# Optimization experiments

Hardware: AMD Instinct MI355X
Metric: run time of the kernel (lower is better)

## Reference

```python
import jax, jax.numpy as jnp
import numpy as np

TEMPERATURE = 30.0
LN_EPS = 1e-5

B, CIN, COUT, S, HID, K = 64, 256, 512, 4096, 64, 4


def setup_inputs() -> dict:
    key = jax.random.key(0)
    ks = jax.random.split(key, 4)
    x = jax.random.normal(ks[0], (B, CIN, S), dtype=jnp.float32)
    w1 = jax.random.normal(ks[1], (HID, CIN), dtype=jnp.float32) * (1.0 / np.sqrt(CIN))
    w2 = jax.random.normal(ks[2], (K, HID), dtype=jnp.float32) * (1.0 / np.sqrt(HID))
    b2 = jnp.zeros((K,), dtype=jnp.float32)
    conv_w = jax.random.normal(ks[3], (K, COUT, CIN), dtype=jnp.float32) * (1.0 / np.sqrt(CIN))
    conv_b = jnp.zeros((K, COUT), dtype=jnp.float32)
    gamma = jnp.ones((S,), dtype=jnp.float32)
    beta = jnp.zeros((S,), dtype=jnp.float32)
    return {"x": x, "w1": w1, "w2": w2, "b2": b2, "conv_w": conv_w,
            "conv_b": conv_b, "gamma": gamma, "beta": beta}


def reference(x, w1, w2, b2, conv_w, conv_b, gamma, beta):
    # --- attention over K kernel experts (global avg pool -> FC -> ReLU -> FC -> softmax/T) ---
    pooled = x.mean(axis=-1)                               # [B, Cin]
    h = jax.nn.relu(pooled @ w1.T)                         # [B, H]
    logits = h @ w2.T + b2                                 # [B, K]
    att = jax.nn.softmax(logits / TEMPERATURE, axis=-1)    # [B, K]
    # --- per-sample mixed 1x1 conv weights (grouped-conv trick == batched matmul) ---
    Wb = jnp.einsum('bk,koi->boi', att, conv_w)            # [B, Cout, Cin]
    bb = att @ conv_b                                      # [B, Cout]
    y = jnp.einsum('boi,bis->bos', Wb, x) + bb[:, :, None]  # [B, Cout, S]
    # --- LayerNorm over time axis (Samples) ---
    mu = y.mean(axis=-1, keepdims=True)
    var = y.var(axis=-1, keepdims=True)
    y = (y - mu) * jax.lax.rsqrt(var + LN_EPS) * gamma + beta
    # --- GELU (torch default: exact erf); dropout is identity in eval mode ---
    return jax.nn.gelu(y, approximate=False)
```

## Files before the change

kernel.cpp:

```cpp
#include <hip/hip_runtime.h>
#include <hip/hip_bf16.h>

#define B_   64
#define CIN  256
#define COUT 512
#define S_   4096
#define HID  64
#define KEXP 4

typedef float f32x4 __attribute__((ext_vector_type(4)));
typedef short bf16x8 __attribute__((ext_vector_type(8)));

static __device__ __forceinline__ unsigned short f2bf(float f) {
    union { float f; unsigned u; } c; c.f = f;
    unsigned r = c.u + 0x7FFFu + ((c.u >> 16) & 1u);
    return (unsigned short)(r >> 16);
}
static __device__ __forceinline__ float bf2f(unsigned short u) {
    union { unsigned u; float f; } c; c.u = ((unsigned)u) << 16;
    return c.f;
}

#define GSTR 68
__global__ __launch_bounds__(512, 2) void k_gram_part(const float* __restrict__ x,
                                                      unsigned short* __restrict__ part,
                                                      float* __restrict__ ppart,
                                                      unsigned short* __restrict__ xF) {
    __shared__ unsigned short lds[256 * GSTR];
    int bid = blockIdx.x;
    int b = bid & 63, sc = bid >> 6;
    int t = threadIdx.x, lane = t & 63, wv = t >> 6;
    int wr = wv >> 1, wc = wv & 1;
    const float* xb = x + (size_t)b * CIN * S_;
    unsigned short* xFb = xF + (size_t)b * S_ * CIN;

    f32x4 acc[4][8] = {};
    float psum[8] = {0.f, 0.f, 0.f, 0.f, 0.f, 0.f, 0.f, 0.f};

    for (int step = 0; step < 16; ++step) {
        int s0 = sc * 1024 + step * 64;
        __syncthreads();
#pragma unroll
        for (int p = 0; p < 8; ++p) {
            int i = t + p * 512;
            int row = i >> 4, f4 = i & 15;
            float4 v = *(const float4*)(xb + (size_t)row * S_ + s0 + f4 * 4);
            psum[p] += v.x + v.y + v.z + v.w;
            unsigned short u[4] = {f2bf(v.x), f2bf(v.y), f2bf(v.z), f2bf(v.w)};
            *(uint2*)&lds[row * GSTR + f4 * 4] = *(const uint2*)u;
        }
        __syncthreads();
        {
#pragma unroll
            for (int it = 0; it < 4; ++it) {
                int slot = t + it * 512;
                int chunk = slot >> 6;
                int st_l = chunk >> 3, kb = chunk & 7;
                int l = slot & 63;
                unsigned short tmp[8];
#pragma unroll
                for (int j = 0; j < 8; ++j)
                    tmp[j] = lds[(kb * 32 + (l >> 4) * 8 + j) * GSTR + st_l * 16 + (l & 15)];
                *(uint4*)(xFb + ((size_t)((s0 >> 4) + st_l) * 8 + kb) * 512 + l * 8) = *(const uint4*)tmp;
            }
        }
#pragma unroll
        for (int kk = 0; kk < 2; ++kk) {
            bf16x8 bfr[8];
#pragma unroll
            for (int nf = 0; nf < 8; ++nf)
                bfr[nf] = *(const bf16x8*)&lds[(wc * 128 + nf * 16 + (lane & 15)) * GSTR + kk * 32 + (lane >> 4) * 8];
#pragma unroll
            for (int mfi = 0; mfi < 4; ++mfi) {
                bf16x8 afr = *(const bf16x8*)&lds[(wr * 64 + mfi * 16 + (lane & 15)) * GSTR + kk * 32 + (lane >> 4) * 8];
#pragma unroll
                for (int nf = 0; nf < 8; ++nf)
                    acc[mfi][nf] = __builtin_amdgcn_mfma_f32_16x16x32_bf16(afr, bfr[nf], acc[mfi][nf], 0, 0, 0);
            }
        }
    }
#pragma unroll
    for (int p = 0; p < 8; ++p) {
        float s = psum[p];
        s += __shfl_xor(s, 1); s += __shfl_xor(s, 2);
        s += __shfl_xor(s, 4); s += __shfl_xor(s, 8);
        if ((t & 15) == 0) ppart[((size_t)sc * 64 + b) * 256 + ((t + p * 512) >> 4)] = s;
    }
    unsigned short* pb = part + ((size_t)sc * 64 + b) * 65536;
#pragma unroll
    for (int mfi = 0; mfi < 4; ++mfi) {
#pragma unroll
        for (int r = 0; r < 4; ++r) {
            int row = wr * 64 + mfi * 16 + (lane >> 4) * 4 + r;
#pragma unroll
            for (int nf = 0; nf < 8; ++nf)
                pb[row * 256 + wc * 128 + nf * 16 + (lane & 15)] = f2bf(acc[mfi][nf][r]);
        }
    }
}

__global__ __launch_bounds__(256) void k_gred(const unsigned short* __restrict__ part,
                                              const float* __restrict__ ppart,
                                              unsigned short* __restrict__ ghat,
                                              float* __restrict__ pooled) {
    int b = blockIdx.x, t = threadIdx.x;
    const size_t bo = (size_t)b * 65536;
    const size_t scs = (size_t)64 * 65536;
    const float inv = 1.f / S_;
    for (int it = 0; it < 32; ++it) {
        size_t i = bo + (size_t)(it * 256 + t) * 8;
        union { uint4 v; unsigned short s[8]; } a0, a1, a2, a3, o;
        a0.v = *(const uint4*)(part + i);
        a1.v = *(const uint4*)(part + scs + i);
        a2.v = *(const uint4*)(part + 2 * scs + i);
        a3.v = *(const uint4*)(part + 3 * scs + i);
#pragma unroll
        for (int j = 0; j < 8; ++j)
            o.s[j] = f2bf((bf2f(a0.s[j]) + bf2f(a1.s[j]) + bf2f(a2.s[j]) + bf2f(a3.s[j])) * inv);
        *(uint4*)&ghat[i] = o.v;
    }
    float p = ppart[(size_t)b * 256 + t] + ppart[(size_t)(64 + b) * 256 + t]
            + ppart[(size_t)(128 + b) * 256 + t] + ppart[(size_t)(192 + b) * 256 + t];
    pooled[b * 256 + t] = p * inv;
}

__global__ __launch_bounds__(64) void k_att(const float* __restrict__ pooled,
                                            const float* __restrict__ w1,
                                            const float* __restrict__ w2,
                                            const float* __restrict__ b2,
                                            float* __restrict__ att_out) {
    int b = blockIdx.x, t = threadIdx.x;
    __shared__ float pl[CIN];
    __shared__ float hl[HID];
    __shared__ float satt[KEXP];
    for (int j = t; j < CIN; j += 64) pl[j] = pooled[b * CIN + j];
    __syncthreads();
    float acc = 0.f;
    const float* w1r = w1 + t * CIN;
#pragma unroll 4
    for (int c = 0; c < CIN; c += 4) {
        float4 w = *(const float4*)(w1r + c);
        acc += w.x * pl[c] + w.y * pl[c + 1] + w.z * pl[c + 2] + w.w * pl[c + 3];
    }
    hl[t] = fmaxf(acc, 0.f);
    __syncthreads();
    if (t < KEXP) {
        float a = 0.f;
        for (int j = 0; j < HID; ++j) a += hl[j] * w2[t * HID + j];
        satt[t] = (a + b2[t]) * (1.0f / 30.0f);
    }
    __syncthreads();
    if (t == 0) {
        float m = fmaxf(fmaxf(satt[0], satt[1]), fmaxf(satt[2], satt[3]));
        float e0 = expf(satt[0] - m), e1 = expf(satt[1] - m);
        float e2 = expf(satt[2] - m), e3 = expf(satt[3] - m);
        float inv = 1.f / (e0 + e1 + e2 + e3);
        att_out[b * KEXP + 0] = e0 * inv;
        att_out[b * KEXP + 1] = e1 * inv;
        att_out[b * KEXP + 2] = e2 * inv;
        att_out[b * KEXP + 3] = e3 * inv;
    }
}

__global__ __launch_bounds__(256) void k_wb(const float* __restrict__ conv_w,
                                            const float* __restrict__ att,
                                            unsigned short* __restrict__ wb) {
    int bid = blockIdx.x;
    int b = bid >> 5, o0 = (bid & 31) * 16;
    int t = threadIdx.x;
    int o = o0 + (t >> 4);
    int i0 = (t & 15) * 16;
    float ak[KEXP];
#pragma unroll
    for (int k = 0; k < KEXP; ++k) ak[k] = att[b * KEXP + k];
    float acc[16];
#pragma unroll
    for (int j = 0; j < 16; ++j) acc[j] = 0.f;
#pragma unroll
    for (int k = 0; k < KEXP; ++k) {
        const float* src = conv_w + ((size_t)(k * COUT + o)) * CIN + i0;
#pragma unroll
        for (int j4 = 0; j4 < 4; ++j4) {
            float4 v = *(const float4*)(src + j4 * 4);
            acc[j4 * 4 + 0] += ak[k] * v.x;
            acc[j4 * 4 + 1] += ak[k] * v.y;
            acc[j4 * 4 + 2] += ak[k] * v.z;
            acc[j4 * 4 + 3] += ak[k] * v.w;
        }
    }
    unsigned short us[16];
#pragma unroll
    for (int j = 0; j < 16; ++j) us[j] = f2bf(acc[j]);
    unsigned short* dst = wb + (size_t)(b * COUT + o) * CIN + i0;
    *(uint4*)(dst) = *(const uint4*)(us);
    *(uint4*)(dst + 8) = *(const uint4*)(us + 8);
}

#define ASTR 264

__global__ __launch_bounds__(256, 2) void k_z(const unsigned short* __restrict__ wb,
                                              const unsigned short* __restrict__ ghat,
                                              float* __restrict__ zout) {
    __shared__ unsigned short lds_a[128 * ASTR];
    int bid = blockIdx.x;
    int b = bid & 63;
    int tile = bid >> 6;
    int m0 = (tile & 3) * 128, n0 = (tile >> 2) * 128;
    int t = threadIdx.x;
    {
        int row = t >> 1, half = t & 1;
        const unsigned short* src = wb + (size_t)(b * COUT + m0 + row) * CIN + half * 128;
        unsigned short* dstrow = &lds_a[row * ASTR + half * 128];
#pragma unroll
        for (int j = 0; j < 16; ++j)
            *(uint4*)(dstrow + j * 8) = *(const uint4*)(src + j * 8);
    }
    __syncthreads();

    int lane = t & 63;
    int wid = t >> 6;
    int arow = lane & 15;
    int kq = lane >> 4;
    int col0 = n0 + wid * 32 + (lane & 15);
    int col1 = col0 + 16;
    const unsigned short* gb = ghat + (size_t)b * 256 * 256;

    f32x4 acc[8][2] = {};
#pragma unroll
    for (int kk = 0; kk < 8; ++kk) {
        bf16x8 b0 = *(const bf16x8*)(gb + (size_t)col0 * 256 + kk * 32 + kq * 8);
        bf16x8 b1 = *(const bf16x8*)(gb + (size_t)col1 * 256 + kk * 32 + kq * 8);
#pragma unroll
        for (int mf = 0; mf < 8; ++mf) {
            int row = mf * 16 + arow;
            bf16x8 a = *(const bf16x8*)&lds_a[row * ASTR + kk * 32 + kq * 8];
            acc[mf][0] = __builtin_amdgcn_mfma_f32_16x16x32_bf16(a, b0, acc[mf][0], 0, 0, 0);
            acc[mf][1] = __builtin_amdgcn_mfma_f32_16x16x32_bf16(a, b1, acc[mf][1], 0, 0, 0);
        }
    }
#pragma unroll
    for (int mf = 0; mf < 8; ++mf) {
#pragma unroll
        for (int r = 0; r < 4; ++r) {
            int row = m0 + mf * 16 + (lane >> 4) * 4 + r;
            size_t rb = ((size_t)b * COUT + row) * 256;
#pragma unroll
            for (int nf = 0; nf < 2; ++nf) {
                int col = n0 + wid * 32 + nf * 16 + (lane & 15);
                zout[rb + col] = acc[mf][nf][r];
            }
        }
    }
}

__global__ __launch_bounds__(256) void k_v(const float* __restrict__ z,
                                           const unsigned short* __restrict__ wb,
                                           const float* __restrict__ pooled,
                                           float* __restrict__ mu,
                                           float* __restrict__ rstd) {
    int gid = blockIdx.x * 4 + (threadIdx.x >> 6);
    int lane = threadIdx.x & 63;
    int b = gid >> 9;
    const float* zr = z + (size_t)gid * 256;
    const unsigned short* wr = wb + (size_t)gid * 256;

    float4 zv = *(const float4*)(zr + lane * 4);
    ushort4 wu = *(const ushort4*)(wr + lane * 4);
    float w0 = bf2f(wu.x), w1 = bf2f(wu.y), w2 = bf2f(wu.z), w3 = bf2f(wu.w);
    float4 pv = *(const float4*)(pooled + b * CIN + lane * 4);

    float v = zv.x * w0 + zv.y * w1 + zv.z * w2 + zv.w * w3;
    float m = pv.x * w0 + pv.y * w1 + pv.z * w2 + pv.w * w3;
#pragma unroll
    for (int off = 1; off < 64; off <<= 1) {
        v += __shfl_xor(v, off);
        m += __shfl_xor(m, off);
    }
    if (lane == 0) {
        float var = v - m * m;
        mu[gid] = m;
        rstd[gid] = rsqrtf(var + 1e-5f);
    }
}

static __device__ __forceinline__ float gelu_t(float z) {
    float d = -1.5957691216f * z * (1.f + 0.044715f * z * z);
    return z * __builtin_amdgcn_rcpf(1.f + __expf(d));
}

static __device__ __forceinline__ void loadB(bf16x8 (&dst)[8], const unsigned short* p) {
#pragma unroll
    for (int kk = 0; kk < 8; ++kk) dst[kk] = *(const bf16x8*)(p + kk * 512);
}

__global__ __launch_bounds__(256) void k_main13(const unsigned short* __restrict__ xF,
                                                const unsigned short* __restrict__ wb,
                                                const float* __restrict__ mu,
                                                const float* __restrict__ rstd,
                                                const float* __restrict__ gamma,
                                                const float* __restrict__ beta,
                                                float* __restrict__ out) {
    int bid = blockIdx.x;
    int xcd = bid & 7;
    int local = bid >> 3;
    int rh = local & 3;
    int sq = (local >> 2) & 3;
    int bq = local >> 4;
    int b = xcd + 8 * bq;

    int t = threadIdx.x, lane = t & 63, w = t >> 6;
    int lm = lane & 15, lk = lane >> 4;
    int row0 = rh * 128 + w * 32;

    bf16x8 A[2][8];
    const unsigned short* wbb = wb + (size_t)(b * COUT + row0 + lm) * CIN + lk * 8;
#pragma unroll
    for (int rf = 0; rf < 2; ++rf)
#pragma unroll
        for (int kk = 0; kk < 8; ++kk)
            A[rf][kk] = *(const bf16x8*)(wbb + (size_t)(rf * 16) * CIN + kk * 32);

    float mu_r[8], rs_r[8];
#pragma unroll
    for (int rf = 0; rf < 2; ++rf)
#pragma unroll
        for (int rr = 0; rr < 4; ++rr) {
            int row = b * COUT + row0 + rf * 16 + lk * 4 + rr;
            mu_r[rf * 4 + rr] = mu[row];
            rs_r[rf * 4 + rr] = rstd[row];
        }

    const float* gq = gamma + sq * 1024;
    const float* bq_ = beta + sq * 1024;
    float* outb = out + (size_t)(b * COUT + row0) * S_ + sq * 1024;
    const unsigned short* xFq = xF + (size_t)b * S_ * CIN + (size_t)sq * 262144 + lane * 8;

    bf16x8 B0[8], B1[8];
    loadB(B0, xFq);

#define STEP(st_, Bc)                                                                        \
    {                                                                                        \
        f32x4 a0 = {0.f, 0.f, 0.f, 0.f}, a1 = {0.f, 0.f, 0.f, 0.f};                         \
        _Pragma("unroll") for (int kk = 0; kk < 8; ++kk) {                                   \
            a0 = __builtin_amdgcn_mfma_f32_16x16x32_bf16(A[0][kk], Bc[kk], a0, 0, 0, 0);     \
            a1 = __builtin_amdgcn_mfma_f32_16x16x32_bf16(A[1][kk], Bc[kk], a1, 0, 0, 0);     \
        }                                                                                    \
        int cloc = (st_) * 16 + lm;                                                          \
        float g = gq[cloc], be = bq_[cloc];                                                  \
        _Pragma("unroll") for (int rr = 0; rr < 4; ++rr) {                                   \
            float z0 = (a0[rr] - mu_r[rr]) * rs_r[rr] * g + be;                              \
            outb[(size_t)(lk * 4 + rr) * S_ + cloc] = gelu_t(z0);                            \
            float z1 = (a1[rr] - mu_r[4 + rr]) * rs_r[4 + rr] * g + be;                      \
            outb[(size_t)(16 + lk * 4 + rr) * S_ + cloc] = gelu_t(z1);                       \
        }                                                                                    \
    }

    for (int st = 0; st < 64; st += 2) {
        loadB(B1, xFq + (size_t)(st + 1) * 4096);
        STEP(st, B0)
        int nn = (st + 2 < 64) ? st + 2 : 63;
        loadB(B0, xFq + (size_t)nn * 4096);
        STEP(st + 1, B1)
    }
#undef STEP
}

extern "C" void kernel_launch(void* const* d_in, const int* in_sizes, int n_in,
                              void* d_out, int out_size, void* d_ws, size_t ws_size,
                              hipStream_t stream) {
    const float* x      = (const float*)d_in[0];
    const float* w1     = (const float*)d_in[1];
    const float* w2     = (const float*)d_in[2];
    const float* b2     = (const float*)d_in[3];
    const float* conv_w = (const float*)d_in[4];
    const float* gamma  = (const float*)d_in[6];
    const float* beta   = (const float*)d_in[7];
    float* out = (float*)d_out;

    float* pooled = (float*)d_ws;
    float* att    = (float*)((char*)d_ws + 65536);
    unsigned short* wb   = (unsigned short*)((char*)d_ws + 262144);
    unsigned short* ghat = (unsigned short*)((char*)d_ws + 17039360);
    float* mu   = (float*)((char*)d_ws + 25427968);
    float* rstd = (float*)((char*)d_ws + 25559040);
    float* ppart = (float*)((char*)d_ws + 25690112);
    unsigned short* xF = (unsigned short*)((char*)d_ws + 33554432);

    unsigned short* part = (unsigned short*)out;
    float* zbuf = (float*)((char*)d_out + 67108864);

    k_gram_part<<<256, 512, 0, stream>>>(x, part, ppart, xF);
    k_gred<<<B_, 256, 0, stream>>>(part, ppart, ghat, pooled);
    k_att<<<B_, 64, 0, stream>>>(pooled, w1, w2, b2, att);
    k_wb<<<B_ * 32, 256, 0, stream>>>(conv_w, att, wb);
    k_z<<<512, 256, 0, stream>>>(wb, ghat, zbuf);
    k_v<<<B_ * COUT / 4, 256, 0, stream>>>(zbuf, wb, pooled, mu, rstd);
    k_main13<<<1024, 256, 0, stream>>>(xF, wb, mu, rstd, gamma, beta, out);
}
```

Measured before the change: 496.8 us.

## Stage xF tiles through LDS ring with direct global-to-LDS loads and vectorized epilogue

Replaces the main fused GEMM+LayerNorm+GELU kernel with a 512-thread, 256-block version. B tiles are loaded asynchronously into a three-slot LDS ring using global_load_lds and shared by all 8 waves, instead of each wave loading its own copy into registers. Results are staged through per-wave LDS scratch so that output stores become coalesced float4 writes, with gamma/beta cached in LDS. This adds a barrier every step and uses more LDS, and it lowers block count and occupancy.

Result: faster. 438.1 us (-11.8%).

```diff
diff --git a/kernel.cpp b/kernel.cpp
--- a/kernel.cpp
+++ b/kernel.cpp
@@ -19,6 +19,13 @@
 static __device__ __forceinline__ float bf2f(unsigned short u) {
     union { unsigned u; float f; } c; c.u = ((unsigned)u) << 16;
     return c.f;
+}
+
+static __device__ __forceinline__ void gl16(const unsigned short* g, unsigned short* l) {
+    __builtin_amdgcn_global_load_lds(
+        (const __attribute__((address_space(1))) void*)g,
+        (__attribute__((address_space(3))) void*)l,
+        16, 0, 0);
 }
 
 #define GSTR 68
@@ -288,29 +295,38 @@
     return z * __builtin_amdgcn_rcpf(1.f + __expf(d));
 }
 
-static __device__ __forceinline__ void loadB(bf16x8 (&dst)[8], const unsigned short* p) {
-#pragma unroll
-    for (int kk = 0; kk < 8; ++kk) dst[kk] = *(const bf16x8*)(p + kk * 512);
-}
-
-__global__ __launch_bounds__(256) void k_main13(const unsigned short* __restrict__ xF,
+#define EPW 66
+__global__ __launch_bounds__(512) void k_main14(const unsigned short* __restrict__ xF,
                                                 const unsigned short* __restrict__ wb,
                                                 const float* __restrict__ mu,
                                                 const float* __restrict__ rstd,
                                                 const float* __restrict__ gamma,
                                                 const float* __restrict__ beta,
                                                 float* __restrict__ out) {
+    __shared__ unsigned short ring[3][8192];
+    __shared__ float eps[8][32 * EPW];
+    __shared__ float gb_lds[2048];
+    __shared__ float be_lds[2048];
+
     int bid = blockIdx.x;
     int xcd = bid & 7;
     int local = bid >> 3;
-    int rh = local & 3;
-    int sq = (local >> 2) & 3;
-    int bq = local >> 4;
+    int rh = local & 1;
+    int sq = (local >> 1) & 1;
+    int bq = local >> 2;
     int b = xcd + 8 * bq;
 
     int t = threadIdx.x, lane = t & 63, w = t >> 6;
     int lm = lane & 15, lk = lane >> 4;
-    int row0 = rh * 128 + w * 32;
+    int row0 = rh * 256 + w * 32;
+    int colbase = sq * 2048;
+
+    {
+        float4 g4 = *(const float4*)(gamma + colbase + t * 4);
+        float4 b4 = *(const float4*)(beta + colbase + t * 4);
+        *(float4*)&gb_lds[t * 4] = g4;
+        *(float4*)&be_lds[t * 4] = b4;
+    }
 
     bf16x8 A[2][8];
     const unsigned short* wbb = wb + (size_t)(b * COUT + row0 + lm) * CIN + lk * 8;
@@ -320,49 +336,86 @@
         for (int kk = 0; kk < 8; ++kk)
             A[rf][kk] = *(const bf16x8*)(wbb + (size_t)(rf * 16) * CIN + kk * 32);
 
-    float mu_r[8], rs_r[8];
-#pragma unroll
-    for (int rf = 0; rf < 2; ++rf)
-#pragma unroll
-        for (int rr = 0; rr < 4; ++rr) {
-            int row = b * COUT + row0 + rf * 16 + lk * 4 + rr;
-            mu_r[rf * 4 + rr] = mu[row];
-            rs_r[rf * 4 + rr] = rstd[row];
-        }
-
-    const float* gq = gamma + sq * 1024;
-    const float* bq_ = beta + sq * 1024;
-    float* outb = out + (size_t)(b * COUT + row0) * S_ + sq * 1024;
-    const unsigned short* xFq = xF + (size_t)b * S_ * CIN + (size_t)sq * 262144 + lane * 8;
-
-    bf16x8 B0[8], B1[8];
-    loadB(B0, xFq);
-
-#define STEP(st_, Bc)                                                                        \
-    {                                                                                        \
-        f32x4 a0 = {0.f, 0.f, 0.f, 0.f}, a1 = {0.f, 0.f, 0.f, 0.f};                         \
-        _Pragma("unroll") for (int kk = 0; kk < 8; ++kk) {                                   \
-            a0 = __builtin_amdgcn_mfma_f32_16x16x32_bf16(A[0][kk], Bc[kk], a0, 0, 0, 0);     \
-            a1 = __builtin_amdgcn_mfma_f32_16x16x32_bf16(A[1][kk], Bc[kk], a1, 0, 0, 0);     \
-        }                                                                                    \
-        int cloc = (st_) * 16 + lm;                                                          \
-        float g = gq[cloc], be = bq_[cloc];                                                  \
-        _Pragma("unroll") for (int rr = 0; rr < 4; ++rr) {                                   \
-            float z0 = (a0[rr] - mu_r[rr]) * rs_r[rr] * g + be;                              \
-            outb[(size_t)(lk * 4 + rr) * S_ + cloc] = gelu_t(z0);                            \
-            float z1 = (a1[rr] - mu_r[4 + rr]) * rs_r[4 + rr] * g + be;                      \
-            outb[(size_t)(16 + lk * 4 + rr) * S_ + cloc] = gelu_t(z1);                       \
-        }                                                                                    \
-    }
-
-    for (int st = 0; st < 64; st += 2) {
-        loadB(B1, xFq + (size_t)(st + 1) * 4096);
-        STEP(st, B0)
-        int nn = (st + 2 < 64) ? st + 2 : 63;
-        loadB(B0, xFq + (size_t)nn * 4096);
-        STEP(st + 1, B1)
-    }
-#undef STEP
+    int r0 = lane >> 3;
+    int c4 = (lane & 7) * 4;
+    float muf[4], rsf[4];
+#pragma unroll
+    for (int j = 0; j < 4; ++j) {
+        int row = b * COUT + row0 + r0 + 8 * j;
+        muf[j] = mu[row];
+        rsf[j] = rstd[row];
+    }
+    float* outb = out + (size_t)(b * COUT + row0) * S_ + colbase;
+    float* epw = &eps[w][0];
+
+    const unsigned short* xFq = xF + (size_t)b * S_ * CIN + (size_t)sq * 524288;
+
+#define STAGE(st_, slot_)                                                          \
+    {                                                                              \
+        gl16(xFq + (size_t)((st_) * 16 + 2 * w) * 512 + lane * 8,                  \
+             &ring[slot_][(2 * w) * 512]);                                         \
+        gl16(xFq + (size_t)((st_) * 16 + 2 * w + 1) * 512 + lane * 8,              \
+             &ring[slot_][(2 * w + 1) * 512]);                                     \
+    }
+
+    STAGE(0, 0)
+    STAGE(1, 1)
+    __syncthreads();
+
+    for (int st = 0; st < 64; ++st) {
+        if (st + 2 < 64) {
+            int sp = st + 2, slot = sp - (sp / 3) * 3;
+            STAGE(sp, slot)
+        }
+
+        const unsigned short* sl = &ring[st - (st / 3) * 3][0];
+        f32x4 acc[2][2] = {};
+#pragma unroll
+        for (int cf = 0; cf < 2; ++cf) {
+            bf16x8 Bf[8];
+#pragma unroll
+            for (int kb = 0; kb < 8; ++kb)
+                Bf[kb] = *(const bf16x8*)(sl + (cf * 8 + kb) * 512 + lane * 8);
+#pragma unroll
+            for (int kb = 0; kb < 8; ++kb) {
+                acc[0][cf] = __builtin_amdgcn_mfma_f32_16x16x32_bf16(A[0][kb], Bf[kb], acc[0][cf], 0, 0, 0);
+                acc[1][cf] = __builtin_amdgcn_mfma_f32_16x16x32_bf16(A[1][kb], Bf[kb], acc[1][cf], 0, 0, 0);
+            }
+        }
+
+#pragma unroll
+        for (int cf = 0; cf < 2; ++cf)
+#pragma unroll
+            for (int rf = 0; rf < 2; ++rf)
+#pragma unroll
+                for (int rr = 0; rr < 4; ++rr)
+                    epw[(rf * 16 + lk * 4 + rr) * EPW + (st & 1) * 32 + cf * 16 + lm] =
+                        acc[rf][cf][rr];
+
+        if (st & 1) {
+            int fg = st >> 1;
+#pragma unroll
+            for (int j = 0; j < 4; ++j) {
+                int rloc = r0 + 8 * j;
+#pragma unroll
+                for (int seg = 0; seg < 2; ++seg) {
+                    int cl = seg * 32 + c4;
+                    float2 lo = *(const float2*)&epw[rloc * EPW + cl];
+                    float2 hi = *(const float2*)&epw[rloc * EPW + cl + 2];
+                    float4 g4 = *(const float4*)&gb_lds[fg * 64 + cl];
+                    float4 b4 = *(const float4*)&be_lds[fg * 64 + cl];
+                    float4 o;
+                    o.x = gelu_t((lo.x - muf[j]) * rsf[j] * g4.x + b4.x);
+                    o.y = gelu_t((lo.y - muf[j]) * rsf[j] * g4.y + b4.y);
+                    o.z = gelu_t((hi.x - muf[j]) * rsf[j] * g4.z + b4.z);
+                    o.w = gelu_t((hi.y - muf[j]) * rsf[j] * g4.w + b4.w);
+                    *(float4*)(outb + (size_t)rloc * S_ + fg * 64 + cl) = o;
+                }
+            }
+        }
+        __syncthreads();
+    }
+#undef STAGE
 }
 
 extern "C" void kernel_launch(void* const* d_in, const int* in_sizes, int n_in,
@@ -395,5 +448,5 @@
     k_wb<<<B_ * 32, 256, 0, stream>>>(conv_w, att, wb);
     k_z<<<512, 256, 0, stream>>>(wb, ghat, zbuf);
     k_v<<<B_ * COUT / 4, 256, 0, stream>>>(zbuf, wb, pooled, mu, rstd);
-    k_main13<<<1024, 256, 0, stream>>>(xF, wb, mu, rstd, gamma, beta, out);
-}
+    k_main14<<<256, 512, 0, stream>>>(xF, wb, mu, rstd, gamma, beta, out);
+}
```
